# Kernel optimization log

Hardware: AMD Instinct MI355X
Metric: run time of the kernel (lower is better)

The kernel has to match this reference:

```python
import jax, jax.numpy as jnp
import numpy as np

NUM_HEADS = 16
SPARSITY = 0.1


def setup_inputs() -> dict:
    key = jax.random.key(0)
    ks = jax.random.split(key, 3)
    B, N, C = 2, 2048, 1024
    x = jax.random.normal(ks[0], (B, N, C), dtype=jnp.float32)
    w_qkv = jax.random.normal(ks[1], (C, 3 * C), dtype=jnp.float32) * 0.02
    b_qkv = jnp.zeros((3 * C,), dtype=jnp.float32)
    w_out = jax.random.normal(ks[2], (C, C), dtype=jnp.float32) * 0.02
    b_out = jnp.zeros((C,), dtype=jnp.float32)
    return {"x": x, "w_qkv": w_qkv, "b_qkv": b_qkv, "w_out": w_out, "b_out": b_out}


def reference(x, w_qkv, b_qkv, w_out, b_out):
    B, N, C = x.shape
    H = NUM_HEADS
    hd = C // H
    scale = hd ** (-0.5)
    # qkv projection: [B,N,3C] -> [3,B,H,N,hd]
    qkv = (x @ w_qkv + b_qkv).reshape(B, N, 3, H, hd).transpose(2, 0, 3, 1, 4)
    q, k, v = qkv[0], qkv[1], qkv[2]
    scores = jnp.einsum('bhnd,bhmd->bhnm', q, k) * scale  # [B,H,N,N]
    k_sparse = int(SPARSITY * N)
    if 0 < k_sparse < N:
        _, idx = jax.lax.top_k(scores, k_sparse)  # [B,H,N,k]
        bi = jnp.arange(B)[:, None, None, None]
        hi = jnp.arange(H)[None, :, None, None]
        ni = jnp.arange(N)[None, None, :, None]
        mask = jnp.zeros_like(scores).at[bi, hi, ni, idx].set(1.0)
        scores = scores * mask - 1e9 * (1.0 - mask)
    attn = jax.nn.softmax(scores, axis=-1)
    out = jnp.einsum('bhnm,bhmd->bhnd', attn, v)  # [B,H,N,hd]
    out = out.transpose(0, 2, 1, 3).reshape(B, N, C)
    return out @ w_out + b_out
```

## Files before the change

### kernel.cpp

```cpp
#include <hip/hip_runtime.h>
#include <cstdint>


#define BB 2
#define NN 2048
#define CC 1024
#define HH 16
#define HD 64
#define KSP 204

typedef _Float16 f16x8v __attribute__((ext_vector_type(8)));

__device__ __forceinline__ unsigned long long mono64(double s) {
  long long bb = __double_as_longlong(s);
  return (unsigned long long)bb ^
         ((bb < 0) ? 0xFFFFFFFFFFFFFFFFull : 0x8000000000000000ull);
}

__global__ __launch_bounds__(256) void qk_gemm_f64(
    const float* __restrict__ x, const float* __restrict__ w,
    const float* __restrict__ bqkv, double* __restrict__ Qd,
    double* __restrict__ Kd) {
  __shared__ double As[16][64];
  __shared__ double Bs[16][64];
  const int tid = threadIdx.x;
  const int tx = tid & 15, ty = tid >> 4;
  const int colbase = blockIdx.x * 64, rowbase = blockIdx.y * 64;

  double acc[4][4] = {};

  const int sr = tid >> 2, sc = (tid & 3) * 4;
  const int bk = tid >> 4, bn = (tid & 15) * 4;

  for (int kt = 0; kt < 64; ++kt) {
    const int k0 = kt * 16;
    const float4 av = *(const float4*)(x + (size_t)(rowbase + sr) * 1024 + k0 + sc);
    const float4 bv = *(const float4*)(w + (size_t)(k0 + bk) * 3072 + colbase + bn);
    __syncthreads();
    As[sc + 0][sr] = (double)av.x;
    As[sc + 1][sr] = (double)av.y;
    As[sc + 2][sr] = (double)av.z;
    As[sc + 3][sr] = (double)av.w;
    Bs[bk][bn + 0] = (double)bv.x;
    Bs[bk][bn + 1] = (double)bv.y;
    Bs[bk][bn + 2] = (double)bv.z;
    Bs[bk][bn + 3] = (double)bv.w;
    __syncthreads();
#pragma unroll
    for (int k = 0; k < 16; ++k) {
      double a[4], b[4];
#pragma unroll
      for (int i = 0; i < 4; ++i) a[i] = As[k][ty + 16 * i];
#pragma unroll
      for (int j = 0; j < 4; ++j) b[j] = Bs[k][tx + 16 * j];
#pragma unroll
      for (int i = 0; i < 4; ++i)
#pragma unroll
        for (int j = 0; j < 4; ++j) acc[i][j] = fma(a[i], b[j], acc[i][j]);
    }
  }

  const int region = colbase >> 10;
#pragma unroll
  for (int j = 0; j < 4; ++j) {
    const int col = colbase + tx + 16 * j;
    const double bias = (double)bqkv[col];
    const int h = (col & 1023) >> 6, d = col & 63;
#pragma unroll
    for (int i = 0; i < 4; ++i) {
      const int row = rowbase + ty + 16 * i;
      const int b = row >> 11, n = row & 2047;
      const size_t o = ((size_t)((b * HH + h) * HD + d)) * NN + n;
      const double v = acc[i][j] + bias;
      if (region == 0)
        Qd[o] = v * 0.125;
      else
        Kd[o] = v;
    }
  }
}

__global__ __launch_bounds__(256) void v_gemm_f32(
    const float* __restrict__ x, const float* __restrict__ w,
    const float* __restrict__ bqkv, float* __restrict__ Vf) {
  __shared__ float As[16][64];
  __shared__ float Bs[16][64];
  const int tid = threadIdx.x;
  const int tx = tid & 15, ty = tid >> 4;
  const int colbase = blockIdx.x * 64, rowbase = blockIdx.y * 64;

  float acc[4][4] = {};

  const int sr = tid >> 2, sc = (tid & 3) * 4;
  const int bk = tid >> 4, bn = (tid & 15) * 4;

  for (int kt = 0; kt < 64; ++kt) {
    const int k0 = kt * 16;
    const float4 av = *(const float4*)(x + (size_t)(rowbase + sr) * 1024 + k0 + sc);
    const float4 bv =
        *(const float4*)(w + (size_t)(k0 + bk) * 3072 + 2048 + colbase + bn);
    __syncthreads();
    As[sc + 0][sr] = av.x;
    As[sc + 1][sr] = av.y;
    As[sc + 2][sr] = av.z;
    As[sc + 3][sr] = av.w;
    Bs[bk][bn + 0] = bv.x;
    Bs[bk][bn + 1] = bv.y;
    Bs[bk][bn + 2] = bv.z;
    Bs[bk][bn + 3] = bv.w;
    __syncthreads();
#pragma unroll
    for (int k = 0; k < 16; ++k) {
      float a[4], b[4];
#pragma unroll
      for (int i = 0; i < 4; ++i) a[i] = As[k][ty + 16 * i];
#pragma unroll
      for (int j = 0; j < 4; ++j) b[j] = Bs[k][tx + 16 * j];
#pragma unroll
      for (int i = 0; i < 4; ++i)
#pragma unroll
        for (int j = 0; j < 4; ++j) acc[i][j] = fmaf(a[i], b[j], acc[i][j]);
    }
  }

#pragma unroll
  for (int j = 0; j < 4; ++j) {
    const int col = colbase + tx + 16 * j;
    const float bias = bqkv[2048 + col];
    const int h = col >> 6, d = col & 63;
#pragma unroll
    for (int i = 0; i < 4; ++i) {
      const int row = rowbase + ty + 16 * i;
      const int b = row >> 11, n = row & 2047;
      Vf[((size_t)((b * HH + h) * HD + d)) * NN + n] = acc[i][j] + bias;
    }
  }
}

__global__ __launch_bounds__(512, 2) void attn_exact(
    const double* __restrict__ Qd, const double* __restrict__ Kd,
    const float* __restrict__ Vf, float* __restrict__ attnv) {
  __shared__ __align__(16) float TS32[8][2048];
  __shared__ __align__(16) double QrowT[64][8];
  __shared__ float Zrow[8];

  _Float16* Pp = (_Float16*)&TS32[0][0];

  const int tid = threadIdx.x;
  const int lane = tid & 63;
  const int w = tid >> 6;

  const int bid = (int)(blockIdx.x & 7) * 1024 + ((int)blockIdx.x >> 3);
  const int bh = bid >> 8;
  const int n0 = (bid & 255) * 8;

  const double* Kbh = Kd + (size_t)bh * HD * NN;

  {
    const int d = tid >> 3, r = tid & 7;
    QrowT[d][r] = Qd[((size_t)bh * HD + d) * NN + n0 + r];
  }
  __syncthreads();

  double acc[8][4];
#pragma unroll
  for (int r = 0; r < 8; ++r)
#pragma unroll
    for (int j = 0; j < 4; ++j) acc[r][j] = 0.0;

  {
    const double* kp = Kbh + w * 256 + 2 * lane;
#pragma unroll 2
    for (int d = 0; d < 64; ++d) {
      const double* kr = kp + (size_t)d * NN;
      const double2 kv0 = *(const double2*)(kr);
      const double2 kv1 = *(const double2*)(kr + 128);
      double q[8];
#pragma unroll
      for (int rp = 0; rp < 4; ++rp)
        *(double2*)&q[rp * 2] = *(const double2*)&QrowT[d][rp * 2];
#pragma unroll
      for (int r = 0; r < 8; ++r) {
        acc[r][0] = fma(q[r], kv0.x, acc[r][0]);
        acc[r][1] = fma(q[r], kv0.y, acc[r][1]);
        acc[r][2] = fma(q[r], kv1.x, acc[r][2]);
        acc[r][3] = fma(q[r], kv1.y, acc[r][3]);
      }
    }
  }

#pragma unroll
  for (int r = 0; r < 8; ++r) {
    float2 t0, t1;
    t0.x = (float)acc[r][0];
    t0.y = (float)acc[r][1];
    t1.x = (float)acc[r][2];
    t1.y = (float)acc[r][3];
    *(float2*)&TS32[r][w * 256 + 2 * lane] = t0;
    *(float2*)&TS32[r][w * 256 + 128 + 2 * lane] = t1;
  }
  __syncthreads();

  unsigned ka[32];
  unsigned selmask = 0;
  float mxf;
  {
    unsigned kmax = 0;
#pragma unroll
    for (int i = 0; i < 32; ++i) {
      const int ib = __float_as_int(TS32[w][lane + 64 * i]);
      ka[i] = (unsigned)ib ^ ((ib < 0) ? 0xFFFFFFFFu : 0x80000000u);
      kmax = (ka[i] > kmax) ? ka[i] : kmax;
    }
#pragma unroll
    for (int m = 1; m < 64; m <<= 1) {
      const unsigned o = __shfl_xor(kmax, m, 64);
      kmax = (o > kmax) ? o : kmax;
    }
    mxf = __int_as_float(
        (int)((kmax & 0x80000000u) ? (kmax ^ 0x80000000u) : ~kmax));

    unsigned T32 = 0;
#pragma unroll 1
    for (int bit = 31; bit >= 0; --bit) {
      const unsigned cand = T32 | (1u << bit);
      int c = 0;
#pragma unroll
      for (int i = 0; i < 32; ++i) c += __popcll(__ballot(ka[i] >= cand));
      if (c >= KSP) T32 = cand;
    }

    int cgt = 0, ceq = 0;
#pragma unroll
    for (int i = 0; i < 32; ++i) {
      cgt += __popcll(__ballot(ka[i] > T32));
      ceq += __popcll(__ballot(ka[i] == T32));
    }

    if (cgt + ceq == KSP) {
#pragma unroll
      for (int i = 0; i < 32; ++i)
        selmask |= (ka[i] >= T32) ? (1u << i) : 0u;
    } else {
      double sv[32];
#pragma unroll
      for (int i = 0; i < 32; ++i) sv[i] = 0.0;
#pragma unroll 1
      for (int d = 0; d < 64; ++d) {
        const double qd = QrowT[d][w];
        const double* kr = Kbh + (size_t)d * NN + lane;
#pragma unroll
        for (int i = 0; i < 32; ++i) sv[i] = fma(qd, kr[64 * i], sv[i]);
      }
      unsigned long long T = 0ull;
#pragma unroll 1
      for (int bit = 63; bit >= 0; --bit) {
        const unsigned long long cand = T | (1ull << bit);
        int c = 0;
#pragma unroll
        for (int i = 0; i < 32; ++i)
          c += __popcll(__ballot(ka[i] == T32 && mono64(sv[i]) >= cand));
        if (cgt + c >= KSP) T = cand;
      }
#pragma unroll
      for (int i = 0; i < 32; ++i)
        selmask |= ((ka[i] > T32) || (ka[i] == T32 && mono64(sv[i]) >= T))
                       ? (1u << i)
                       : 0u;
    }
  }
  __syncthreads();

  {
    float z = 0.f;
#pragma unroll
    for (int i = 0; i < 32; ++i) {
      const float f = __int_as_float(
          (int)((ka[i] & 0x80000000u) ? (ka[i] ^ 0x80000000u) : ~ka[i]));
      const float p = ((selmask >> i) & 1u) ? __expf(f - mxf) : 0.0f;
      Pp[(lane + 64 * i) * 8 + w] = (_Float16)p;
      z += p;
    }
#pragma unroll
    for (int m = 1; m < 64; m <<= 1) z += __shfl_xor(z, m, 64);
    if (lane == 0) Zrow[w] = z;
  }
  __syncthreads();

  const int b2 = bh >> 4, h2 = bh & 15;
#define PV_HALF(H)                                                            \
  {                                                                           \
    float s[4][8];                                                            \
    _Pragma("unroll") for (int d4 = 0; d4 < 4; ++d4)                          \
        _Pragma("unroll") for (int r = 0; r < 8; ++r) s[d4][r] = 0.f;         \
    const float* vb = Vf + ((size_t)bh * HD + 8 * w + (H)*4) * NN;            \
    _Pragma("unroll 2") for (int i = 0; i < 32; ++i) {                        \
      const int k = lane + 64 * i;                                            \
      const f16x8v pk = *(const f16x8v*)&Pp[k * 8];                           \
      float pf[8];                                                            \
      _Pragma("unroll") for (int r = 0; r < 8; ++r) pf[r] = (float)pk[r];     \
      float vv[4];                                                            \
      _Pragma("unroll") for (int d4 = 0; d4 < 4; ++d4) vv[d4] =               \
          vb[(size_t)d4 * NN + k];                                            \
      _Pragma("unroll") for (int d4 = 0; d4 < 4; ++d4)                        \
          _Pragma("unroll") for (int r = 0; r < 8; ++r) s[d4][r] =            \
              fmaf(pf[r], vv[d4], s[d4][r]);                                  \
    }                                                                         \
    _Pragma("unroll") for (int d4 = 0; d4 < 4; ++d4)                          \
        _Pragma("unroll") for (int r = 0; r < 8; ++r) {                       \
      float v = s[d4][r];                                                     \
      _Pragma("unroll") for (int m = 1; m < 64; m <<= 1) v +=                 \
          __shfl_xor(v, m, 64);                                               \
      if (lane == 0)                                                          \
        attnv[((size_t)(b2 * NN + n0 + r)) * CC + h2 * HD + 8 * w + (H)*4 +   \
              d4] = v / Zrow[r];                                              \
    }                                                                         \
  }

  PV_HALF(0)
  PV_HALF(1)
}

__global__ __launch_bounds__(256) void out_gemm_f32(
    const float* __restrict__ A, const float* __restrict__ W,
    const float* __restrict__ bout, float* __restrict__ out) {
  __shared__ float As[16][64];
  __shared__ float Bs[16][64];
  const int tid = threadIdx.x;
  const int tx = tid & 15, ty = tid >> 4;
  const int colbase = blockIdx.x * 64, rowbase = blockIdx.y * 64;

  float acc[4][4] = {};

  const int sr = tid >> 2, sc = (tid & 3) * 4;
  const int bk = tid >> 4, bn = (tid & 15) * 4;

  for (int kt = 0; kt < 64; ++kt) {
    const int k0 = kt * 16;
    const float4 av = *(const float4*)(A + (size_t)(rowbase + sr) * 1024 + k0 + sc);
    const float4 bv = *(const float4*)(W + (size_t)(k0 + bk) * 1024 + colbase + bn);
    __syncthreads();
    As[sc + 0][sr] = av.x;
    As[sc + 1][sr] = av.y;
    As[sc + 2][sr] = av.z;
    As[sc + 3][sr] = av.w;
    Bs[bk][bn + 0] = bv.x;
    Bs[bk][bn + 1] = bv.y;
    Bs[bk][bn + 2] = bv.z;
    Bs[bk][bn + 3] = bv.w;
    __syncthreads();
#pragma unroll
    for (int k = 0; k < 16; ++k) {
      float a[4], b[4];
#pragma unroll
      for (int i = 0; i < 4; ++i) a[i] = As[k][ty + 16 * i];
#pragma unroll
      for (int j = 0; j < 4; ++j) b[j] = Bs[k][tx + 16 * j];
#pragma unroll
      for (int i = 0; i < 4; ++i)
#pragma unroll
        for (int j = 0; j < 4; ++j) acc[i][j] = fmaf(a[i], b[j], acc[i][j]);
    }
  }

#pragma unroll
  for (int j = 0; j < 4; ++j) {
    const int col = colbase + tx + 16 * j;
    const float bias = bout[col];
#pragma unroll
    for (int i = 0; i < 4; ++i) {
      const int row = rowbase + ty + 16 * i;
      out[(size_t)row * CC + col] = acc[i][j] + bias;
    }
  }
}

extern "C" void kernel_launch(void* const* d_in, const int* in_sizes, int n_in,
                              void* d_out, int out_size, void* d_ws,
                              size_t ws_size, hipStream_t stream) {
  const float* x     = (const float*)d_in[0];
  const float* w_qkv = (const float*)d_in[1];
  const float* b_qkv = (const float*)d_in[2];
  const float* w_out = (const float*)d_in[3];
  const float* b_out = (const float*)d_in[4];
  float* out = (float*)d_out;

  char* ws = (char*)d_ws;
  const size_t SZ_QD = (size_t)BB * HH * HD * NN * 8;
  const size_t SZ_VF = (size_t)BB * HH * HD * NN * 4;
  const size_t SZ_AT = (size_t)4096 * 1024 * 4;

  size_t off = 0;
  double* Qd    = (double*)(ws + off); off += SZ_QD;
  double* Kd    = (double*)(ws + off); off += SZ_QD;
  float*  Vf    = (float*)(ws + off);  off += SZ_VF;
  float*  attnv = (float*)(ws + off);  off += SZ_AT;

  {
    dim3 g(2048 / 64, 4096 / 64);
    qk_gemm_f64<<<g, 256, 0, stream>>>(x, w_qkv, b_qkv, Qd, Kd);
  }
  {
    dim3 g(1024 / 64, 4096 / 64);
    v_gemm_f32<<<g, 256, 0, stream>>>(x, w_qkv, b_qkv, Vf);
  }
  attn_exact<<<BB * HH * (NN / 8), 512, 0, stream>>>(Qd, Kd, Vf, attnv);
  {
    dim3 g(1024 / 64, 4096 / 64);
    out_gemm_f32<<<g, 256, 0, stream>>>(attnv, w_out, b_out, out);
  }
}
```

Before: 1.941 ms.

## Prefetch next GEMM tiles into registers and store probabilities as fp32 in place

All three tiled GEMMs now load the next k-tile from global memory into registers right after the shared-memory store, so the load overlaps the current tile's FMA loop. In the attention kernel, the fp16 interleaved probability buffer and one __syncthreads are dropped. Each wave writes its fp32 probabilities straight into its own TS32 row, and the PV loop reads them back as fp32. The QK^T loop unroll also goes from 2 to 4. This trades extra registers and possible occupancy loss, plus eight scalar LDS reads in place of one vector read, for latency hiding and no fp16 rounding.

```diff
diff --git a/kernel.cpp b/kernel.cpp
--- a/kernel.cpp
+++ b/kernel.cpp
@@ -8,8 +8,6 @@
 #define HH 16
 #define HD 64
 #define KSP 204
-
-typedef _Float16 f16x8v __attribute__((ext_vector_type(8)));
 
 __device__ __forceinline__ unsigned long long mono64(double s) {
   long long bb = __double_as_longlong(s);
@@ -32,10 +30,13 @@
   const int sr = tid >> 2, sc = (tid & 3) * 4;
   const int bk = tid >> 4, bn = (tid & 15) * 4;
 
+  const float* pa = x + (size_t)(rowbase + sr) * 1024 + sc;
+  const float* pb = w + (size_t)bk * 3072 + colbase + bn;
+
+  float4 av = *(const float4*)(pa);
+  float4 bv = *(const float4*)(pb);
+
   for (int kt = 0; kt < 64; ++kt) {
-    const int k0 = kt * 16;
-    const float4 av = *(const float4*)(x + (size_t)(rowbase + sr) * 1024 + k0 + sc);
-    const float4 bv = *(const float4*)(w + (size_t)(k0 + bk) * 3072 + colbase + bn);
     __syncthreads();
     As[sc + 0][sr] = (double)av.x;
     As[sc + 1][sr] = (double)av.y;
@@ -46,6 +47,10 @@
     Bs[bk][bn + 2] = (double)bv.z;
     Bs[bk][bn + 3] = (double)bv.w;
     __syncthreads();
+    if (kt < 63) {
+      av = *(const float4*)(pa + (kt + 1) * 16);
+      bv = *(const float4*)(pb + (size_t)(kt + 1) * 16 * 3072);
+    }
 #pragma unroll
     for (int k = 0; k < 16; ++k) {
       double a[4], b[4];
@@ -94,11 +99,13 @@
   const int sr = tid >> 2, sc = (tid & 3) * 4;
   const int bk = tid >> 4, bn = (tid & 15) * 4;
 
+  const float* pa = x + (size_t)(rowbase + sr) * 1024 + sc;
+  const float* pb = w + (size_t)bk * 3072 + 2048 + colbase + bn;
+
+  float4 av = *(const float4*)(pa);
+  float4 bv = *(const float4*)(pb);
+
   for (int kt = 0; kt < 64; ++kt) {
-    const int k0 = kt * 16;
-    const float4 av = *(const float4*)(x + (size_t)(rowbase + sr) * 1024 + k0 + sc);
-    const float4 bv =
-        *(const float4*)(w + (size_t)(k0 + bk) * 3072 + 2048 + colbase + bn);
     __syncthreads();
     As[sc + 0][sr] = av.x;
     As[sc + 1][sr] = av.y;
@@ -109,6 +116,10 @@
     Bs[bk][bn + 2] = bv.z;
     Bs[bk][bn + 3] = bv.w;
     __syncthreads();
+    if (kt < 63) {
+      av = *(const float4*)(pa + (kt + 1) * 16);
+      bv = *(const float4*)(pb + (size_t)(kt + 1) * 16 * 3072);
+    }
 #pragma unroll
     for (int k = 0; k < 16; ++k) {
       float a[4], b[4];
@@ -144,8 +155,6 @@
   __shared__ __align__(16) double QrowT[64][8];
   __shared__ float Zrow[8];
 
-  _Float16* Pp = (_Float16*)&TS32[0][0];
-
   const int tid = threadIdx.x;
   const int lane = tid & 63;
   const int w = tid >> 6;
@@ -170,7 +179,7 @@
 
   {
     const double* kp = Kbh + w * 256 + 2 * lane;
-#pragma unroll 2
+#pragma unroll 4
     for (int d = 0; d < 64; ++d) {
       const double* kr = kp + (size_t)d * NN;
       const double2 kv0 = *(const double2*)(kr);
@@ -201,10 +210,10 @@
   }
   __syncthreads();
 
-  unsigned ka[32];
-  unsigned selmask = 0;
-  float mxf;
-  {
+  {
+    unsigned ka[32];
+    unsigned selmask = 0;
+    float mxf;
     unsigned kmax = 0;
 #pragma unroll
     for (int i = 0; i < 32; ++i) {
@@ -268,17 +277,14 @@
                        ? (1u << i)
                        : 0u;
     }
-  }
-  __syncthreads();
-
-  {
+
     float z = 0.f;
 #pragma unroll
     for (int i = 0; i < 32; ++i) {
       const float f = __int_as_float(
           (int)((ka[i] & 0x80000000u) ? (ka[i] ^ 0x80000000u) : ~ka[i]));
       const float p = ((selmask >> i) & 1u) ? __expf(f - mxf) : 0.0f;
-      Pp[(lane + 64 * i) * 8 + w] = (_Float16)p;
+      TS32[w][lane + 64 * i] = p;
       z += p;
     }
 #pragma unroll
@@ -296,9 +302,8 @@
     const float* vb = Vf + ((size_t)bh * HD + 8 * w + (H)*4) * NN;            \
     _Pragma("unroll 2") for (int i = 0; i < 32; ++i) {                        \
       const int k = lane + 64 * i;                                            \
-      const f16x8v pk = *(const f16x8v*)&Pp[k * 8];                           \
       float pf[8];                                                            \
-      _Pragma("unroll") for (int r = 0; r < 8; ++r) pf[r] = (float)pk[r];     \
+      _Pragma("unroll") for (int r = 0; r < 8; ++r) pf[r] = TS32[r][k];       \
       float vv[4];                                                            \
       _Pragma("unroll") for (int d4 = 0; d4 < 4; ++d4) vv[d4] =               \
           vb[(size_t)d4 * NN + k];                                            \
@@ -335,10 +340,13 @@
   const int sr = tid >> 2, sc = (tid & 3) * 4;
   const int bk = tid >> 4, bn = (tid & 15) * 4;
 
+  const float* pa = A + (size_t)(rowbase + sr) * 1024 + sc;
+  const float* pb = W + (size_t)bk * 1024 + colbase + bn;
+
+  float4 av = *(const float4*)(pa);
+  float4 bv = *(const float4*)(pb);
+
   for (int kt = 0; kt < 64; ++kt) {
-    const int k0 = kt * 16;
-    const float4 av = *(const float4*)(A + (size_t)(rowbase + sr) * 1024 + k0 + sc);
-    const float4 bv = *(const float4*)(W + (size_t)(k0 + bk) * 1024 + colbase + bn);
     __syncthreads();
     As[sc + 0][sr] = av.x;
     As[sc + 1][sr] = av.y;
@@ -349,6 +357,10 @@
     Bs[bk][bn + 2] = bv.z;
     Bs[bk][bn + 3] = bv.w;
     __syncthreads();
+    if (kt < 63) {
+      av = *(const float4*)(pa + (kt + 1) * 16);
+      bv = *(const float4*)(pb + (size_t)(kt + 1) * 16 * 1024);
+    }
 #pragma unroll
     for (int k = 0; k < 16; ++k) {
       float a[4], b[4];
```

After: 2.519 ms. +29.8%, slower.
